# Kernel tuning notes

Hardware: AMD Instinct MI355X
Metric: run time of the kernel (lower is better)

Reference implementation:

```python
import jax, jax.numpy as jnp
import numpy as np

EPS = 1e-5  # BatchNorm eps (eval mode, uses running stats)


def _conv1x1(x, W, b):
    # x: [B,C,H,W], W: [O,C], b: [O] -> [B,O,H,W]
    return jnp.einsum('bchw,oc->bohw', x, W) + b[None, :, None, None]


def setup_inputs() -> dict:
    key = jax.random.key(0)
    ks = jax.random.split(key, 13)
    B, C, M, N = 16, 512, 64, 64
    CR = C // 2
    s = 0.02
    return {
        'x': jax.random.normal(ks[0], (B, C, M, N), dtype=jnp.float32),
        'Wq': jax.random.normal(ks[1], (CR, C), dtype=jnp.float32) * s,
        'bq': jax.random.normal(ks[2], (CR,), dtype=jnp.float32) * s,
        'Wk': jax.random.normal(ks[3], (CR, C), dtype=jnp.float32) * s,
        'bk': jax.random.normal(ks[4], (CR,), dtype=jnp.float32) * s,
        'Wv': jax.random.normal(ks[5], (CR, C), dtype=jnp.float32) * s,
        'bv': jax.random.normal(ks[6], (CR,), dtype=jnp.float32) * s,
        'Wr': jax.random.normal(ks[7], (C, CR), dtype=jnp.float32) * s,
        'br': jax.random.normal(ks[8], (C,), dtype=jnp.float32) * s,
        'gamma': jax.random.normal(ks[9], (C,), dtype=jnp.float32) * 0.1 + 1.0,
        'beta': jax.random.normal(ks[10], (C,), dtype=jnp.float32) * 0.1,
        'running_mean': jax.random.normal(ks[11], (C,), dtype=jnp.float32) * 0.1,
        'running_var': jax.random.uniform(ks[12], (C,), dtype=jnp.float32, minval=0.5, maxval=1.5),
    }


def reference(x, Wq, bq, Wk, bk, Wv, bv, Wr, br, gamma, beta, running_mean, running_var):
    b, c, m, n = x.shape
    cr = Wq.shape[0]
    # 1x1-conv QKV projections
    Q = _conv1x1(x, Wq, bq).reshape(b * cr, m, n)
    K = _conv1x1(x, Wk, bk).reshape(b * cr, m, n)
    V = _conv1x1(x, Wv, bv).reshape(b * cr, m, n)
    # per-channel spatial attention over rows: [b*cr, m, m]
    corr = jnp.einsum('gik,gjk->gij', Q, K)
    attn = jax.nn.softmax(corr, axis=-1)
    y = jnp.einsum('gij,gjn->gin', attn, V).reshape(b, cr, m, n)
    # reconstruct: 1x1 conv + BatchNorm (eval mode) + residual
    y = _conv1x1(y, Wr, br)
    inv = gamma / jnp.sqrt(running_var + EPS)
    y = y * inv[None, :, None, None] + (beta - running_mean * inv)[None, :, None, None]
    return y + x
```

## Files before the change

### kernel.cpp

```cpp
#include <hip/hip_runtime.h>

typedef __attribute__((ext_vector_type(8))) short bf16x8;
typedef __attribute__((ext_vector_type(4))) float f32x4;

#define DEVI static __device__ __forceinline__

DEVI unsigned short f2b(float f) {
  union { float f; unsigned u; } v; v.f = f;
  unsigned r = v.u + 0x7fffu + ((v.u >> 16) & 1u);
  return (unsigned short)(r >> 16);
}

typedef const __attribute__((address_space(1))) void* gas1_t;
typedef __attribute__((address_space(3))) void* las3_t;
#define GL16(g, l) __builtin_amdgcn_global_load_lds((gas1_t)(g), (las3_t)(l), 16, 0, 0)

#define WAITVM(N) asm volatile("s_waitcnt vmcnt(" #N ")" ::: "memory")
#define WAITLGKM  asm volatile("s_waitcnt lgkmcnt(0)" ::: "memory")

#define OFF_WQKV  0ull
#define OFF_WR    786432ull
#define OFF_BQKV  1048576ull
#define OFF_SCALE 1051648ull
#define OFF_OFF2  1053696ull
#define OFF_XT    2097152ull
#define OFF_YT    2097152ull
#define OFF_Y     35651584ull
#define OFF_Q     69206016ull

__global__ __launch_bounds__(256) void k_prep(
    const float* __restrict__ Wq, const float* __restrict__ bq,
    const float* __restrict__ Wk, const float* __restrict__ bk,
    const float* __restrict__ Wv, const float* __restrict__ bv,
    const float* __restrict__ Wr, const float* __restrict__ br,
    const float* __restrict__ gamma, const float* __restrict__ beta,
    const float* __restrict__ rm, const float* __restrict__ rv,
    unsigned short* __restrict__ wqkv, unsigned short* __restrict__ wrb,
    float* __restrict__ bqkv, float* __restrict__ scale, float* __restrict__ off2)
{
  int i = blockIdx.x * 256 + threadIdx.x;
  if (i < 768 * 512) {
    int o = i >> 9, c = i & 511;
    float v = (o < 256) ? Wq[o * 512 + c] : (o < 512 ? Wk[(o - 256) * 512 + c] : Wv[(o - 512) * 512 + c]);
    wqkv[i] = f2b(v);
  }
  if (i < 512 * 256) wrb[i] = f2b(Wr[i]);
  if (i < 768) bqkv[i] = (i < 256) ? bq[i] : (i < 512 ? bk[i - 256] : bv[i - 512]);
  if (i < 512) {
    float inv = gamma[i] * rsqrtf(rv[i] + 1e-5f);
    scale[i] = inv;
    off2[i] = (br[i] - rm[i]) * inv + beta[i];
  }
}

__global__ __launch_bounds__(256) void k_xt(const float* __restrict__ x, unsigned short* __restrict__ xt)
{
  __shared__ unsigned short tile[64][72];
  const int b = blockIdx.z, c0 = blockIdx.y * 64, s0 = blockIdx.x * 64;
  const int t = threadIdx.x;
  const int r = t >> 2, cc = (t & 3) * 16;
  const float* src = x + ((size_t)b * 512 + c0 + r) * 4096 + s0 + cc;
  #pragma unroll
  for (int j = 0; j < 16; j += 4) {
    float4 v = *(const float4*)(src + j);
    tile[r][cc + j + 0] = f2b(v.x);
    tile[r][cc + j + 1] = f2b(v.y);
    tile[r][cc + j + 2] = f2b(v.z);
    tile[r][cc + j + 3] = f2b(v.w);
  }
  __syncthreads();
  unsigned short* dst = xt + ((size_t)b * 4096 + s0 + r) * 512 + c0 + cc;
  bf16x8 o0, o1;
  #pragma unroll
  for (int j = 0; j < 8; ++j) { o0[j] = tile[cc + j][r]; o1[j] = tile[cc + 8 + j][r]; }
  *(bf16x8*)(dst) = o0;
  *(bf16x8*)(dst + 8) = o1;
}


__global__ __launch_bounds__(256) void k_qkv(
    const unsigned short* __restrict__ xt, const unsigned short* __restrict__ wqkv,
    const float* __restrict__ bqkv, unsigned short* __restrict__ qkv)
{
  __shared__ unsigned short lds[2][2][8192];
  const int b = blockIdx.z, o0 = blockIdx.y * 128, s0 = blockIdx.x * 128;
  const int t = threadIdx.x, w = t >> 6, l = t & 63;
  const int wm = w >> 1, wn = w & 1, lr = l & 15;
  const int lkE = (l >> 4) * 8;
  const int swE = (lr & 7) * 8;
  const int cp = (t & 7) ^ ((t >> 3) & 7);

  const unsigned short* Ag = wqkv + (size_t)(o0 + (t >> 3)) * 512 + cp * 8;
  const unsigned short* Bg = xt + ((size_t)b * 4096 + s0 + (t >> 3)) * 512 + cp * 8;

  const f32x4 z = {0.f, 0.f, 0.f, 0.f};
  f32x4 acc[4][4];
  #pragma unroll
  for (int i = 0; i < 4; ++i)
    #pragma unroll
    for (int j = 0; j < 4; ++j) acc[i][j] = z;

#define STG_Q(st, kt) do { \
    _Pragma("unroll") \
    for (int j = 0; j < 4; ++j) { \
      GL16(Ag + (kt) * 64 + j * 32 * 512, (char*)&lds[st][0][0] + j * 4096 + t * 16); \
      GL16(Bg + (kt) * 64 + j * 32 * 512, (char*)&lds[st][1][0] + j * 4096 + t * 16); \
    } \
  } while (0)

#define CMP_Q(st) do { \
    const unsigned short* A  = &lds[st][0][0]; \
    const unsigned short* Bl = &lds[st][1][0]; \
    _Pragma("unroll") \
    for (int kc = 0; kc < 2; ++kc) { \
      const int kidx = (kc * 32 + lkE) ^ swE; \
      bf16x8 af[4], bfr[4]; \
      _Pragma("unroll") \
      for (int mi = 0; mi < 4; ++mi) af[mi] = *(const bf16x8*)(A + (wm * 64 + mi * 16 + lr) * 64 + kidx); \
      _Pragma("unroll") \
      for (int ni = 0; ni < 4; ++ni) bfr[ni] = *(const bf16x8*)(Bl + (wn * 64 + ni * 16 + lr) * 64 + kidx); \
      _Pragma("unroll") \
      for (int mi = 0; mi < 4; ++mi) \
        _Pragma("unroll") \
        for (int ni = 0; ni < 4; ++ni) \
          acc[mi][ni] = __builtin_amdgcn_mfma_f32_16x16x32_bf16(af[mi], bfr[ni], acc[mi][ni], 0, 0, 0); \
    } \
    WAITLGKM; __builtin_amdgcn_sched_barrier(0); \
  } while (0)

  STG_Q(0, 0); STG_Q(1, 1);
  #pragma unroll
  for (int kt = 0; kt < 7; ++kt) {
    WAITVM(8);
    __builtin_amdgcn_s_barrier();
    CMP_Q(kt & 1);
    if (kt + 2 < 8) {
      __builtin_amdgcn_s_barrier();
      STG_Q(kt & 1, kt + 2);
    }
  }
  WAITVM(0);
  __builtin_amdgcn_s_barrier();
  CMP_Q(1);

  #pragma unroll
  for (int mi = 0; mi < 4; ++mi) {
    #pragma unroll
    for (int reg = 0; reg < 4; ++reg) {
      const int o = o0 + wm * 64 + mi * 16 + (l >> 4) * 4 + reg;
      const float bias = bqkv[o];
      const size_t base = (size_t)(o >> 8) * 16777216ull + ((size_t)b * 256 + (o & 255)) * 4096;
      #pragma unroll
      for (int ni = 0; ni < 4; ++ni) {
        const int s = s0 + wn * 64 + ni * 16 + lr;
        qkv[base + s] = f2b(acc[mi][ni][reg] + bias);
      }
    }
  }
#undef STG_Q
#undef CMP_Q
}

__global__ __launch_bounds__(256) void k_attn(const unsigned short* __restrict__ qkv,
                                              unsigned short* __restrict__ yout)
{
  __shared__ unsigned short Vt[64][80];
  __shared__ unsigned short P[4][16][80];
  const int g = blockIdx.x;
  const unsigned short* qg = qkv + (size_t)g * 4096;
  const unsigned short* kg = qkv + 16777216ull + (size_t)g * 4096;
  const unsigned short* vg = qkv + 33554432ull + (size_t)g * 4096;
  const int t = threadIdx.x, w = t >> 6, l = t & 63;
  const int lr = l & 15, lk = (l >> 4) * 8;

  {
    const int j = t >> 2, c0 = (t & 3) * 16;
    bf16x8 a = *(const bf16x8*)(vg + j * 64 + c0);
    bf16x8 bb = *(const bf16x8*)(vg + j * 64 + c0 + 8);
    #pragma unroll
    for (int jj = 0; jj < 8; ++jj) { Vt[c0 + jj][j] = a[jj]; Vt[c0 + 8 + jj][j] = bb[jj]; }
  }

  const f32x4 z = {0.f, 0.f, 0.f, 0.f};
  bf16x8 qf[2];
  #pragma unroll
  for (int kc = 0; kc < 2; ++kc) qf[kc] = *(const bf16x8*)(qg + (w * 16 + lr) * 64 + kc * 32 + lk);
  f32x4 accS[4] = {z, z, z, z};
  #pragma unroll
  for (int jt = 0; jt < 4; ++jt)
    #pragma unroll
    for (int kc = 0; kc < 2; ++kc) {
      bf16x8 kf = *(const bf16x8*)(kg + (jt * 16 + lr) * 64 + kc * 32 + lk);
      accS[jt] = __builtin_amdgcn_mfma_f32_16x16x32_bf16(qf[kc], kf, accS[jt], 0, 0, 0);
    }

  #pragma unroll
  for (int reg = 0; reg < 4; ++reg) {
    float mx = fmaxf(fmaxf(accS[0][reg], accS[1][reg]), fmaxf(accS[2][reg], accS[3][reg]));
    #pragma unroll
    for (int m = 1; m < 16; m <<= 1) mx = fmaxf(mx, __shfl_xor(mx, m, 64));
    float e0 = __expf(accS[0][reg] - mx), e1 = __expf(accS[1][reg] - mx);
    float e2 = __expf(accS[2][reg] - mx), e3 = __expf(accS[3][reg] - mx);
    float sm = e0 + e1 + e2 + e3;
    #pragma unroll
    for (int m = 1; m < 16; m <<= 1) sm += __shfl_xor(sm, m, 64);
    const float rs = 1.f / sm;
    const int row = (l >> 4) * 4 + reg;
    P[w][row][0 * 16 + lr] = f2b(e0 * rs);
    P[w][row][1 * 16 + lr] = f2b(e1 * rs);
    P[w][row][2 * 16 + lr] = f2b(e2 * rs);
    P[w][row][3 * 16 + lr] = f2b(e3 * rs);
  }
  __syncthreads();

  bf16x8 pf[2];
  #pragma unroll
  for (int kc = 0; kc < 2; ++kc) pf[kc] = *(const bf16x8*)(&P[w][lr][kc * 32 + lk]);
  f32x4 accY[4] = {z, z, z, z};
  #pragma unroll
  for (int nt = 0; nt < 4; ++nt)
    #pragma unroll
    for (int kc = 0; kc < 2; ++kc) {
      bf16x8 vf = *(const bf16x8*)(&Vt[nt * 16 + lr][kc * 32 + lk]);
      accY[nt] = __builtin_amdgcn_mfma_f32_16x16x32_bf16(pf[kc], vf, accY[nt], 0, 0, 0);
    }

  unsigned short* yg = yout + (size_t)g * 4096;
  #pragma unroll
  for (int nt = 0; nt < 4; ++nt)
    #pragma unroll
    for (int reg = 0; reg < 4; ++reg) {
      const int i = w * 16 + (l >> 4) * 4 + reg;
      yg[i * 64 + nt * 16 + lr] = f2b(accY[nt][reg]);
    }
}

__global__ __launch_bounds__(256) void k_yt(const unsigned short* __restrict__ y, unsigned short* __restrict__ yt)
{
  __shared__ unsigned short tile[64][72];
  const int b = blockIdx.z, cr0 = blockIdx.y * 64, s0 = blockIdx.x * 64;
  const int t = threadIdx.x, r = t >> 2, c0 = (t & 3) * 16;
  const unsigned short* src = y + ((size_t)b * 256 + cr0 + r) * 4096 + s0 + c0;
  bf16x8 a = *(const bf16x8*)(src);
  bf16x8 bb = *(const bf16x8*)(src + 8);
  #pragma unroll
  for (int j = 0; j < 8; ++j) { tile[r][c0 + j] = a[j]; tile[r][c0 + 8 + j] = bb[j]; }
  __syncthreads();
  unsigned short* dst = yt + ((size_t)b * 4096 + s0 + r) * 256 + cr0 + c0;
  bf16x8 o0, o1;
  #pragma unroll
  for (int j = 0; j < 8; ++j) { o0[j] = tile[c0 + j][r]; o1[j] = tile[c0 + 8 + j][r]; }
  *(bf16x8*)(dst) = o0;
  *(bf16x8*)(dst + 8) = o1;
}

__global__ __launch_bounds__(256) void k_recon(
    const unsigned short* __restrict__ yt, const unsigned short* __restrict__ wrb,
    const float* __restrict__ scale, const float* __restrict__ off2,
    const float* __restrict__ x, float* __restrict__ out)
{
  __shared__ unsigned short lds[2][2][8192];
  const int b = blockIdx.z, o0 = blockIdx.y * 128, s0 = blockIdx.x * 128;
  const int t = threadIdx.x, w = t >> 6, l = t & 63;
  const int wm = w >> 1, wn = w & 1, lr = l & 15;
  const int lkE = (l >> 4) * 8;
  const int swE = (lr & 7) * 8;
  const int cp = (t & 7) ^ ((t >> 3) & 7);

  const unsigned short* Ag = wrb + (size_t)(o0 + (t >> 3)) * 256 + cp * 8;
  const unsigned short* Bg = yt + ((size_t)b * 4096 + s0 + (t >> 3)) * 256 + cp * 8;

  const f32x4 z = {0.f, 0.f, 0.f, 0.f};
  f32x4 acc[4][4];
  #pragma unroll
  for (int i = 0; i < 4; ++i)
    #pragma unroll
    for (int j = 0; j < 4; ++j) acc[i][j] = z;

#define STG_R(st, kt) do { \
    _Pragma("unroll") \
    for (int j = 0; j < 4; ++j) { \
      GL16(Ag + (kt) * 64 + j * 32 * 256, (char*)&lds[st][0][0] + j * 4096 + t * 16); \
      GL16(Bg + (kt) * 64 + j * 32 * 256, (char*)&lds[st][1][0] + j * 4096 + t * 16); \
    } \
  } while (0)

#define CMP_R(st) do { \
    const unsigned short* A  = &lds[st][0][0]; \
    const unsigned short* Bl = &lds[st][1][0]; \
    _Pragma("unroll") \
    for (int kc = 0; kc < 2; ++kc) { \
      const int kidx = (kc * 32 + lkE) ^ swE; \
      bf16x8 af[4], bfr[4]; \
      _Pragma("unroll") \
      for (int mi = 0; mi < 4; ++mi) af[mi] = *(const bf16x8*)(A + (wm * 64 + mi * 16 + lr) * 64 + kidx); \
      _Pragma("unroll") \
      for (int ni = 0; ni < 4; ++ni) bfr[ni] = *(const bf16x8*)(Bl + (wn * 64 + ni * 16 + lr) * 64 + kidx); \
      _Pragma("unroll") \
      for (int mi = 0; mi < 4; ++mi) \
        _Pragma("unroll") \
        for (int ni = 0; ni < 4; ++ni) \
          acc[mi][ni] = __builtin_amdgcn_mfma_f32_16x16x32_bf16(af[mi], bfr[ni], acc[mi][ni], 0, 0, 0); \
    } \
    WAITLGKM; __builtin_amdgcn_sched_barrier(0); \
  } while (0)

  STG_R(0, 0); STG_R(1, 1);
  #pragma unroll
  for (int kt = 0; kt < 3; ++kt) {
    WAITVM(8);
    __builtin_amdgcn_s_barrier();
    CMP_R(kt & 1);
    if (kt + 2 < 4) {
      __builtin_amdgcn_s_barrier();
      STG_R(kt & 1, kt + 2);
    }
  }
  WAITVM(0);
  __builtin_amdgcn_s_barrier();
  CMP_R(1);

  #pragma unroll
  for (int mi = 0; mi < 4; ++mi) {
    #pragma unroll
    for (int reg = 0; reg < 4; ++reg) {
      const int o = o0 + wm * 64 + mi * 16 + (l >> 4) * 4 + reg;
      const float sc = scale[o], of = off2[o];
      const size_t base = ((size_t)b * 512 + o) * 4096;
      #pragma unroll
      for (int ni = 0; ni < 4; ++ni) {
        const int s = s0 + wn * 64 + ni * 16 + lr;
        const size_t idx = base + s;
        out[idx] = acc[mi][ni][reg] * sc + of + x[idx];
      }
    }
  }
#undef STG_R
#undef CMP_R
}

extern "C" void kernel_launch(void* const* d_in, const int* in_sizes, int n_in,
                              void* d_out, int out_size, void* d_ws, size_t ws_size,
                              hipStream_t stream)
{
  const float* x     = (const float*)d_in[0];
  const float* Wq    = (const float*)d_in[1];
  const float* bq    = (const float*)d_in[2];
  const float* Wk    = (const float*)d_in[3];
  const float* bk    = (const float*)d_in[4];
  const float* Wv    = (const float*)d_in[5];
  const float* bv    = (const float*)d_in[6];
  const float* Wr    = (const float*)d_in[7];
  const float* br    = (const float*)d_in[8];
  const float* gamma = (const float*)d_in[9];
  const float* beta  = (const float*)d_in[10];
  const float* rm    = (const float*)d_in[11];
  const float* rv    = (const float*)d_in[12];

  char* ws = (char*)d_ws;
  unsigned short* wqkv  = (unsigned short*)(ws + OFF_WQKV);
  unsigned short* wrb   = (unsigned short*)(ws + OFF_WR);
  float* bqkv  = (float*)(ws + OFF_BQKV);
  float* scale = (float*)(ws + OFF_SCALE);
  float* off2  = (float*)(ws + OFF_OFF2);
  unsigned short* xt  = (unsigned short*)(ws + OFF_XT);
  unsigned short* yt  = (unsigned short*)(ws + OFF_YT);
  unsigned short* yb  = (unsigned short*)(ws + OFF_Y);
  unsigned short* qkv = (unsigned short*)(ws + OFF_Q);
  float* out = (float*)d_out;

  hipLaunchKernelGGL(k_prep, dim3(1536), dim3(256), 0, stream,
                     Wq, bq, Wk, bk, Wv, bv, Wr, br, gamma, beta, rm, rv,
                     wqkv, wrb, bqkv, scale, off2);
  hipLaunchKernelGGL(k_xt, dim3(64, 8, 16), dim3(256), 0, stream, x, xt);
  hipLaunchKernelGGL(k_qkv, dim3(32, 6, 16), dim3(256), 0, stream, xt, wqkv, bqkv, qkv);
  hipLaunchKernelGGL(k_attn, dim3(4096), dim3(256), 0, stream, qkv, yb);
  hipLaunchKernelGGL(k_yt, dim3(64, 4, 16), dim3(256), 0, stream, yb, yt);
  hipLaunchKernelGGL(k_recon, dim3(32, 4, 16), dim3(256), 0, stream, yt, wrb, scale, off2, x, out);
}
```

Before: 212.5 us.

## Fuse weight prep into transpose kernel, remap GEMM blocks by XCD, raise MFMA priority

Merges the weight/bias conversion kernel into the x transpose kernel, removing one launch. The QKV and reconstruct GEMMs switch to a 1D grid whose block index is remapped so consecutive tiles land on the same XCD, aiming at better L2 reuse. Their compute macros now load both k-chunks of fragments before issuing all MFMAs under raised wave priority (s_setprio), and the in-loop sync now always issues a second barrier with explicit sched barriers. The attention MFMAs also get raised priority. Dropping the explicit lgkmcnt wait leans on the compiler to insert the waits for the LDS reads the MFMAs consume.

```diff
diff --git a/kernel.cpp b/kernel.cpp
--- a/kernel.cpp
+++ b/kernel.cpp
@@ -17,6 +17,7 @@
 
 #define WAITVM(N) asm volatile("s_waitcnt vmcnt(" #N ")" ::: "memory")
 #define WAITLGKM  asm volatile("s_waitcnt lgkmcnt(0)" ::: "memory")
+#define SCHEDBAR  __builtin_amdgcn_sched_barrier(0)
 
 #define OFF_WQKV  0ull
 #define OFF_WR    786432ull
@@ -28,7 +29,8 @@
 #define OFF_Y     35651584ull
 #define OFF_Q     69206016ull
 
-__global__ __launch_bounds__(256) void k_prep(
+__global__ __launch_bounds__(256) void k_xt(
+    const float* __restrict__ x, unsigned short* __restrict__ xt,
     const float* __restrict__ Wq, const float* __restrict__ bq,
     const float* __restrict__ Wk, const float* __restrict__ bk,
     const float* __restrict__ Wv, const float* __restrict__ bv,
@@ -38,26 +40,27 @@
     unsigned short* __restrict__ wqkv, unsigned short* __restrict__ wrb,
     float* __restrict__ bqkv, float* __restrict__ scale, float* __restrict__ off2)
 {
-  int i = blockIdx.x * 256 + threadIdx.x;
-  if (i < 768 * 512) {
-    int o = i >> 9, c = i & 511;
-    float v = (o < 256) ? Wq[o * 512 + c] : (o < 512 ? Wk[(o - 256) * 512 + c] : Wv[(o - 512) * 512 + c]);
-    wqkv[i] = f2b(v);
-  }
-  if (i < 512 * 256) wrb[i] = f2b(Wr[i]);
-  if (i < 768) bqkv[i] = (i < 256) ? bq[i] : (i < 512 ? bk[i - 256] : bv[i - 512]);
-  if (i < 512) {
-    float inv = gamma[i] * rsqrtf(rv[i] + 1e-5f);
-    scale[i] = inv;
-    off2[i] = (br[i] - rm[i]) * inv + beta[i];
-  }
-}
-
-__global__ __launch_bounds__(256) void k_xt(const float* __restrict__ x, unsigned short* __restrict__ xt)
-{
   __shared__ unsigned short tile[64][72];
+  const int t = threadIdx.x;
+  const int bid = blockIdx.x + blockIdx.y * 64 + blockIdx.z * 512;
+
+  if (bid < 1536) {
+    int i = bid * 256 + t;
+    if (i < 768 * 512) {
+      int o = i >> 9, c = i & 511;
+      float v = (o < 256) ? Wq[o * 512 + c] : (o < 512 ? Wk[(o - 256) * 512 + c] : Wv[(o - 512) * 512 + c]);
+      wqkv[i] = f2b(v);
+    }
+    if (i < 512 * 256) wrb[i] = f2b(Wr[i]);
+    if (i < 768) bqkv[i] = (i < 256) ? bq[i] : (i < 512 ? bk[i - 256] : bv[i - 512]);
+    if (i < 512) {
+      float inv = gamma[i] * rsqrtf(rv[i] + 1e-5f);
+      scale[i] = inv;
+      off2[i] = (br[i] - rm[i]) * inv + beta[i];
+    }
+  }
+
   const int b = blockIdx.z, c0 = blockIdx.y * 64, s0 = blockIdx.x * 64;
-  const int t = threadIdx.x;
   const int r = t >> 2, cc = (t & 3) * 16;
   const float* src = x + ((size_t)b * 512 + c0 + r) * 4096 + s0 + cc;
   #pragma unroll
@@ -77,13 +80,15 @@
   *(bf16x8*)(dst + 8) = o1;
 }
 
-
 __global__ __launch_bounds__(256) void k_qkv(
     const unsigned short* __restrict__ xt, const unsigned short* __restrict__ wqkv,
     const float* __restrict__ bqkv, unsigned short* __restrict__ qkv)
 {
   __shared__ unsigned short lds[2][2][8192];
-  const int b = blockIdx.z, o0 = blockIdx.y * 128, s0 = blockIdx.x * 128;
+  const int wg = (blockIdx.x & 7) * 384 + (blockIdx.x >> 3);
+  const int o0 = (wg % 6) * 128;
+  const int s0 = ((wg / 6) & 31) * 128;
+  const int b  = wg / 192;
   const int t = threadIdx.x, w = t >> 6, l = t & 63;
   const int wm = w >> 1, wn = w & 1, lr = l & 15;
   const int lkE = (l >> 4) * 8;
@@ -111,36 +116,37 @@
 #define CMP_Q(st) do { \
     const unsigned short* A  = &lds[st][0][0]; \
     const unsigned short* Bl = &lds[st][1][0]; \
+    bf16x8 af[2][4], bfr[2][4]; \
     _Pragma("unroll") \
     for (int kc = 0; kc < 2; ++kc) { \
       const int kidx = (kc * 32 + lkE) ^ swE; \
-      bf16x8 af[4], bfr[4]; \
-      _Pragma("unroll") \
-      for (int mi = 0; mi < 4; ++mi) af[mi] = *(const bf16x8*)(A + (wm * 64 + mi * 16 + lr) * 64 + kidx); \
-      _Pragma("unroll") \
-      for (int ni = 0; ni < 4; ++ni) bfr[ni] = *(const bf16x8*)(Bl + (wn * 64 + ni * 16 + lr) * 64 + kidx); \
+      _Pragma("unroll") \
+      for (int mi = 0; mi < 4; ++mi) af[kc][mi] = *(const bf16x8*)(A + (wm * 64 + mi * 16 + lr) * 64 + kidx); \
+      _Pragma("unroll") \
+      for (int ni = 0; ni < 4; ++ni) bfr[kc][ni] = *(const bf16x8*)(Bl + (wn * 64 + ni * 16 + lr) * 64 + kidx); \
+    } \
+    __builtin_amdgcn_s_setprio(1); \
+    _Pragma("unroll") \
+    for (int kc = 0; kc < 2; ++kc) \
       _Pragma("unroll") \
       for (int mi = 0; mi < 4; ++mi) \
         _Pragma("unroll") \
         for (int ni = 0; ni < 4; ++ni) \
-          acc[mi][ni] = __builtin_amdgcn_mfma_f32_16x16x32_bf16(af[mi], bfr[ni], acc[mi][ni], 0, 0, 0); \
-    } \
-    WAITLGKM; __builtin_amdgcn_sched_barrier(0); \
+          acc[mi][ni] = __builtin_amdgcn_mfma_f32_16x16x32_bf16(af[kc][mi], bfr[kc][ni], acc[mi][ni], 0, 0, 0); \
+    __builtin_amdgcn_s_setprio(0); \
   } while (0)
 
   STG_Q(0, 0); STG_Q(1, 1);
   #pragma unroll
   for (int kt = 0; kt < 7; ++kt) {
     WAITVM(8);
-    __builtin_amdgcn_s_barrier();
+    __builtin_amdgcn_s_barrier(); SCHEDBAR;
     CMP_Q(kt & 1);
-    if (kt + 2 < 8) {
-      __builtin_amdgcn_s_barrier();
-      STG_Q(kt & 1, kt + 2);
-    }
+    __builtin_amdgcn_s_barrier(); SCHEDBAR;
+    if (kt + 2 < 8) STG_Q(kt & 1, kt + 2);
   }
   WAITVM(0);
-  __builtin_amdgcn_s_barrier();
+  __builtin_amdgcn_s_barrier(); SCHEDBAR;
   CMP_Q(1);
 
   #pragma unroll
@@ -186,6 +192,7 @@
   #pragma unroll
   for (int kc = 0; kc < 2; ++kc) qf[kc] = *(const bf16x8*)(qg + (w * 16 + lr) * 64 + kc * 32 + lk);
   f32x4 accS[4] = {z, z, z, z};
+  __builtin_amdgcn_s_setprio(1);
   #pragma unroll
   for (int jt = 0; jt < 4; ++jt)
     #pragma unroll
@@ -193,6 +200,7 @@
       bf16x8 kf = *(const bf16x8*)(kg + (jt * 16 + lr) * 64 + kc * 32 + lk);
       accS[jt] = __builtin_amdgcn_mfma_f32_16x16x32_bf16(qf[kc], kf, accS[jt], 0, 0, 0);
     }
+  __builtin_amdgcn_s_setprio(0);
 
   #pragma unroll
   for (int reg = 0; reg < 4; ++reg) {
@@ -217,6 +225,7 @@
   #pragma unroll
   for (int kc = 0; kc < 2; ++kc) pf[kc] = *(const bf16x8*)(&P[w][lr][kc * 32 + lk]);
   f32x4 accY[4] = {z, z, z, z};
+  __builtin_amdgcn_s_setprio(1);
   #pragma unroll
   for (int nt = 0; nt < 4; ++nt)
     #pragma unroll
@@ -224,6 +233,7 @@
       bf16x8 vf = *(const bf16x8*)(&Vt[nt * 16 + lr][kc * 32 + lk]);
       accY[nt] = __builtin_amdgcn_mfma_f32_16x16x32_bf16(pf[kc], vf, accY[nt], 0, 0, 0);
     }
+  __builtin_amdgcn_s_setprio(0);
 
   unsigned short* yg = yout + (size_t)g * 4096;
   #pragma unroll
@@ -260,7 +270,10 @@
     const float* __restrict__ x, float* __restrict__ out)
 {
   __shared__ unsigned short lds[2][2][8192];
-  const int b = blockIdx.z, o0 = blockIdx.y * 128, s0 = blockIdx.x * 128;
+  const int wg = (blockIdx.x & 7) * 256 + (blockIdx.x >> 3);
+  const int o0 = (wg % 4) * 128;
+  const int s0 = ((wg / 4) & 31) * 128;
+  const int b  = wg / 128;
   const int t = threadIdx.x, w = t >> 6, l = t & 63;
   const int wm = w >> 1, wn = w & 1, lr = l & 15;
   const int lkE = (l >> 4) * 8;
@@ -288,36 +301,37 @@
 #define CMP_R(st) do { \
     const unsigned short* A  = &lds[st][0][0]; \
     const unsigned short* Bl = &lds[st][1][0]; \
+    bf16x8 af[2][4], bfr[2][4]; \
     _Pragma("unroll") \
     for (int kc = 0; kc < 2; ++kc) { \
       const int kidx = (kc * 32 + lkE) ^ swE; \
-      bf16x8 af[4], bfr[4]; \
-      _Pragma("unroll") \
-      for (int mi = 0; mi < 4; ++mi) af[mi] = *(const bf16x8*)(A + (wm * 64 + mi * 16 + lr) * 64 + kidx); \
-      _Pragma("unroll") \
-      for (int ni = 0; ni < 4; ++ni) bfr[ni] = *(const bf16x8*)(Bl + (wn * 64 + ni * 16 + lr) * 64 + kidx); \
+      _Pragma("unroll") \
+      for (int mi = 0; mi < 4; ++mi) af[kc][mi] = *(const bf16x8*)(A + (wm * 64 + mi * 16 + lr) * 64 + kidx); \
+      _Pragma("unroll") \
+      for (int ni = 0; ni < 4; ++ni) bfr[kc][ni] = *(const bf16x8*)(Bl + (wn * 64 + ni * 16 + lr) * 64 + kidx); \
+    } \
+    __builtin_amdgcn_s_setprio(1); \
+    _Pragma("unroll") \
+    for (int kc = 0; kc < 2; ++kc) \
       _Pragma("unroll") \
       for (int mi = 0; mi < 4; ++mi) \
         _Pragma("unroll") \
         for (int ni = 0; ni < 4; ++ni) \
-          acc[mi][ni] = __builtin_amdgcn_mfma_f32_16x16x32_bf16(af[mi], bfr[ni], acc[mi][ni], 0, 0, 0); \
-    } \
-    WAITLGKM; __builtin_amdgcn_sched_barrier(0); \
+          acc[mi][ni] = __builtin_amdgcn_mfma_f32_16x16x32_bf16(af[kc][mi], bfr[kc][ni], acc[mi][ni], 0, 0, 0); \
+    __builtin_amdgcn_s_setprio(0); \
   } while (0)
 
   STG_R(0, 0); STG_R(1, 1);
   #pragma unroll
   for (int kt = 0; kt < 3; ++kt) {
     WAITVM(8);
-    __builtin_amdgcn_s_barrier();
+    __builtin_amdgcn_s_barrier(); SCHEDBAR;
     CMP_R(kt & 1);
-    if (kt + 2 < 4) {
-      __builtin_amdgcn_s_barrier();
-      STG_R(kt & 1, kt + 2);
-    }
+    __builtin_amdgcn_s_barrier(); SCHEDBAR;
+    if (kt + 2 < 4) STG_R(kt & 1, kt + 2);
   }
   WAITVM(0);
-  __builtin_amdgcn_s_barrier();
+  __builtin_amdgcn_s_barrier(); SCHEDBAR;
   CMP_R(1);
 
   #pragma unroll
@@ -369,12 +383,11 @@
   unsigned short* qkv = (unsigned short*)(ws + OFF_Q);
   float* out = (float*)d_out;
 
-  hipLaunchKernelGGL(k_prep, dim3(1536), dim3(256), 0, stream,
-                     Wq, bq, Wk, bk, Wv, bv, Wr, br, gamma, beta, rm, rv,
+  hipLaunchKernelGGL(k_xt, dim3(64, 8, 16), dim3(256), 0, stream,
+                     x, xt, Wq, bq, Wk, bk, Wv, bv, Wr, br, gamma, beta, rm, rv,
                      wqkv, wrb, bqkv, scale, off2);
-  hipLaunchKernelGGL(k_xt, dim3(64, 8, 16), dim3(256), 0, stream, x, xt);
-  hipLaunchKernelGGL(k_qkv, dim3(32, 6, 16), dim3(256), 0, stream, xt, wqkv, bqkv, qkv);
+  hipLaunchKernelGGL(k_qkv, dim3(3072), dim3(256), 0, stream, xt, wqkv, bqkv, qkv);
   hipLaunchKernelGGL(k_attn, dim3(4096), dim3(256), 0, stream, qkv, yb);
   hipLaunchKernelGGL(k_yt, dim3(64, 4, 16), dim3(256), 0, stream, yb, yt);
-  hipLaunchKernelGGL(k_recon, dim3(32, 4, 16), dim3(256), 0, stream, yt, wrb, scale, off2, x, out);
-}
+  hipLaunchKernelGGL(k_recon, dim3(2048), dim3(256), 0, stream, yt, wrb, scale, off2, x, out);
+}
```

Measured after the change: 215.3 us. Within noise of the previous version (+1.3%).
